# Kernel optimization log

Measured on AMD Instinct MI355X. Metric: run time of the kernel, lower is better.

The kernel has to match this reference:

```python
import jax, jax.numpy as jnp
import numpy as np
from jax import lax

B, H, W = 16, 256, 256
NUM_HIDDEN = 12
C = 3 + NUM_HIDDEN + 1  # 16 channels: rgb + hidden + alpha
HID = 64
ALPHA = 1.0
THR = 0.1

SOBEL_X = jnp.array([[-1.0, 0.0, 1.0], [-2.0, 0.0, 2.0], [-1.0, 0.0, 1.0]], jnp.float32) / 8.0
SOBEL_Y = jnp.array([[-1.0, -2.0, -1.0], [0.0, 0.0, 0.0], [1.0, 2.0, 1.0]], jnp.float32) / 8.0


def _sobel_conv(s, k):
    # s: [B,H,W] channel-summed state; k: [3,3]. SAME-padded 2D stencil.
    return lax.conv_general_dilated(
        s[..., None], k[:, :, None, None], window_strides=(1, 1), padding='SAME',
        dimension_numbers=('NHWC', 'HWIO', 'NHWC'))  # [B,H,W,1]


def _alive(x, thr):
    # 3x3 max-pool over alpha channel (index 3), SAME padding.
    a = x[..., 3:4]
    pooled = lax.reduce_window(a, -jnp.inf, lax.max, (1, 3, 3, 1), (1, 1, 1, 1), 'SAME')
    return pooled > thr  # [B,H,W,1] bool


def setup_inputs() -> dict:
    key = jax.random.key(0)
    ks = jax.random.split(key, 7)
    x = jax.random.uniform(ks[0], (B, H, W, C), dtype=jnp.float32)
    # UpdateNet params: 1x1 convs stored as dense matrices [in, out].
    w1 = jax.random.normal(ks[1], (3 * C, HID), dtype=jnp.float32) * (1.0 / np.sqrt(3 * C))
    b1 = jnp.zeros((HID,), jnp.float32)
    w2 = jax.random.normal(ks[2], (HID, HID), dtype=jnp.float32) * (1.0 / np.sqrt(HID))
    b2 = jnp.zeros((HID,), jnp.float32)
    # Original zero-inits w3; use small random values so outputs/grads are nontrivial.
    w3 = jax.random.normal(ks[3], (HID, C), dtype=jnp.float32) * 0.01
    return {'x': x, 'w1': w1, 'b1': b1, 'w2': w2, 'b2': b2, 'w3': w3}


def reference(x, w1, b1, w2, b2, w3):
    pre_life = _alive(x, THR)
    # Sobel perception: kernel[o,i] = sobel for all o,i  =>  each output channel
    # is the sobel filter applied to the channel-sum; broadcast across C channels.
    s = jnp.sum(x, axis=-1)                      # [B,H,W]
    sx = _sobel_conv(s, SOBEL_X)                 # [B,H,W,1]
    sy = _sobel_conv(s, SOBEL_Y)                 # [B,H,W,1]
    perc = jnp.concatenate(
        [x, jnp.broadcast_to(sx, x.shape), jnp.broadcast_to(sy, x.shape)], axis=-1)  # [B,H,W,3C]
    # UpdateNet: two biased 1x1 convs + ReLU, then unbiased 1x1 conv.
    h = jax.nn.relu(jnp.einsum('bhwi,io->bhwo', perc, w1) + b1)
    h = jax.nn.relu(jnp.einsum('bhwi,io->bhwo', h, w2) + b2)
    update = jnp.einsum('bhwi,io->bhwo', h, w3)  # [B,H,W,C]
    # cell_fire_rate == 1.0 -> stochastic update mask is all ones.
    x_new = x + ALPHA * update
    post_life = _alive(x_new, THR)
    life = (pre_life & post_life).astype(x_new.dtype)
    return x_new * life
```

## Files before the change

### kernel.cpp

```cpp
#include <hip/hip_runtime.h>
#include <hip/hip_bf16.h>
#include <cstdint>

#define NPIX (16 * 256 * 256)
#define THRV 0.1f

typedef __bf16 bf16x8 __attribute__((ext_vector_type(8)));
typedef float  f32x4  __attribute__((ext_vector_type(4)));

#define NSLOT 18

__global__ __launch_bounds__(256) void k_prep(const float* __restrict__ x,
                                              const float* __restrict__ w1,
                                              const float* __restrict__ b1,
                                              const float* __restrict__ w2,
                                              const float* __restrict__ b2,
                                              const float* __restrict__ w3,
                                              float2* __restrict__ hxs,
                                              unsigned char* __restrict__ rpre,
                                              float4* __restrict__ wpack) {
    __shared__ float sS[258];
    __shared__ float sA[258];
    const int tid = threadIdx.x;
    const int p = blockIdx.x * 256 + tid;

    const float4* xp = (const float4*)(x + (size_t)p * 16);
    float4 a = xp[0], b = xp[1], c = xp[2], d = xp[3];
    float sum = ((a.x + a.y) + (a.z + a.w)) + ((b.x + b.y) + (b.z + b.w)) +
                ((c.x + c.y) + (c.z + c.w)) + ((d.x + d.y) + (d.z + d.w));
    sS[tid + 1] = sum;
    sA[tid + 1] = a.w;
    if (tid == 0) { sS[0] = 0.f; sS[257] = 0.f; sA[0] = -1e30f; sA[257] = -1e30f; }
    __syncthreads();

    hxs[p] = make_float2(sS[tid + 2] - sS[tid],
                         sS[tid] + 2.f * sS[tid + 1] + sS[tid + 2]);
    float rm = fmaxf(sA[tid], fmaxf(sA[tid + 1], sA[tid + 2]));
    rpre[p] = (rm > THRV) ? 1 : 0;

    if (blockIdx.x == 0 && tid < 64) {
        const int lane = tid;
        const int r = lane & 15, g = lane >> 4;
#pragma unroll
        for (int n = 0; n < 4; ++n) {
            const int cc = n * 16 + r;
            bf16x8 f;
#pragma unroll
            for (int j = 0; j < 8; ++j) {
                float v = 0.f;
                if (j < 4) v = w1[(g * 4 + j) * 64 + cc];
                else if (g == 0 && j == 4) { for (int t = 0; t < 16; ++t) v += w1[(16 + t) * 64 + cc]; }
                else if (g == 0 && j == 5) { for (int t = 0; t < 16; ++t) v += w1[(32 + t) * 64 + cc]; }
                else if (g == 1 && j == 4) v = b1[cc];
                f[j] = (__bf16)v;
            }
            wpack[n * 64 + lane] = *(const float4*)&f;
        }
#pragma unroll
        for (int s = 0; s < 2; ++s)
#pragma unroll
            for (int n = 0; n < 4; ++n) {
                bf16x8 f;
#pragma unroll
                for (int j = 0; j < 8; ++j) {
                    const int psi = (2 * s + (j >> 2)) * 16 + g * 4 + (j & 3);
                    f[j] = (__bf16)w2[psi * 64 + n * 16 + r];
                }
                wpack[(4 + s * 4 + n) * 64 + lane] = *(const float4*)&f;
            }
#pragma unroll
        for (int s = 0; s < 2; ++s) {
            bf16x8 f;
#pragma unroll
            for (int j = 0; j < 8; ++j) {
                const int psi = (2 * s + (j >> 2)) * 16 + g * 4 + (j & 3);
                f[j] = (__bf16)w3[psi * 16 + r];
            }
            wpack[(12 + s) * 64 + lane] = *(const float4*)&f;
        }
#pragma unroll
        for (int n = 0; n < 4; ++n) {
            f32x4 v;
#pragma unroll
            for (int q = 0; q < 4; ++q) v[q] = b2[n * 16 + g * 4 + q];
            wpack[(14 + n) * 64 + lane] = *(const float4*)&v;
        }
    }
}

__global__ __launch_bounds__(256) void k_mfma(const float* __restrict__ x,
                                              const float2* __restrict__ hxs,
                                              const float4* __restrict__ wpack,
                                              float* __restrict__ out,
                                              unsigned char* __restrict__ anewf) {
    const int tid = threadIdx.x;
    const int wv = tid >> 6, lane = tid & 63;
    const int r = lane & 15, g = lane >> 4;

    bf16x8 w1f[4], w2f[2][4], w3f[2];
    f32x4 b2v[4];
#pragma unroll
    for (int n = 0; n < 4; ++n) { float4 t = wpack[n * 64 + lane]; w1f[n] = *(bf16x8*)&t; }
#pragma unroll
    for (int s2 = 0; s2 < 2; ++s2)
#pragma unroll
        for (int n = 0; n < 4; ++n) { float4 t = wpack[(4 + s2 * 4 + n) * 64 + lane]; w2f[s2][n] = *(bf16x8*)&t; }
#pragma unroll
    for (int s2 = 0; s2 < 2; ++s2) { float4 t = wpack[(12 + s2) * 64 + lane]; w3f[s2] = *(bf16x8*)&t; }
#pragma unroll
    for (int n = 0; n < 4; ++n) { float4 t = wpack[(14 + n) * 64 + lane]; b2v[n] = *(f32x4*)&t; }

    const int row = (blockIdx.x & 7) * 512 + (blockIdx.x >> 3);
    const int y = row & 255;
    const size_t rbase = (size_t)row * 256;
    const int wcol = wv * 64;

    const int y2 = y + g - 1;
    const bool gok = (g < 3) & ((unsigned)y2 < 256u);
    const size_t hbase = ((rbase >> 8) << 8) * 1 + ((size_t)(row >> 8) << 16);
    const float2* hrow = hxs + ((size_t)(row >> 8) << 16) + (size_t)(gok ? y2 : 0) * 256;

    float4 xf[4]; float2 hv[4];
#pragma unroll
    for (int t = 0; t < 4; ++t) {
        const int col = wcol + t * 16 + r;
        xf[t] = *(const float4*)(x + (rbase + col) * 16 + g * 4);
        hv[t] = gok ? hrow[col] : make_float2(0.f, 0.f);
    }

#pragma unroll
    for (int t = 0; t < 4; ++t) {
        const int col = wcol + t * 16 + r;
        const size_t pix = rbase + col;

        float ax = hv[t].x * ((g == 1) ? 2.f : 1.f);
        float ay = (g == 2) ? hv[t].y : ((g == 0) ? -hv[t].y : 0.f);
        ax += __shfl_xor(ax, 16); ax += __shfl_xor(ax, 32);
        ay += __shfl_xor(ay, 16); ay += __shfl_xor(ay, 32);
        const float gx = ax * 0.125f;
        const float gy = ay * 0.125f;

        bf16x8 a1;
        a1[0] = (__bf16)xf[t].x; a1[1] = (__bf16)xf[t].y;
        a1[2] = (__bf16)xf[t].z; a1[3] = (__bf16)xf[t].w;
        a1[4] = (__bf16)(g == 0 ? gx : (g == 1 ? 1.f : 0.f));
        a1[5] = (__bf16)(g == 0 ? gy : 0.f);
        a1[6] = (__bf16)0.f; a1[7] = (__bf16)0.f;

        f32x4 acc1[4];
#pragma unroll
        for (int n = 0; n < 4; ++n)
            acc1[n] = __builtin_amdgcn_mfma_f32_16x16x32_bf16(
                w1f[n], a1, (f32x4){0.f, 0.f, 0.f, 0.f}, 0, 0, 0);

        bf16x8 bf2[2];
#pragma unroll
        for (int s2 = 0; s2 < 2; ++s2)
#pragma unroll
            for (int j = 0; j < 4; ++j) {
                bf2[s2][j]     = (__bf16)fmaxf(acc1[2 * s2][j], 0.f);
                bf2[s2][4 + j] = (__bf16)fmaxf(acc1[2 * s2 + 1][j], 0.f);
            }

        f32x4 acc2[4];
#pragma unroll
        for (int n = 0; n < 4; ++n) {
            acc2[n] = b2v[n];
            acc2[n] = __builtin_amdgcn_mfma_f32_16x16x32_bf16(w2f[0][n], bf2[0], acc2[n], 0, 0, 0);
            acc2[n] = __builtin_amdgcn_mfma_f32_16x16x32_bf16(w2f[1][n], bf2[1], acc2[n], 0, 0, 0);
        }

        bf16x8 bf3[2];
#pragma unroll
        for (int s2 = 0; s2 < 2; ++s2)
#pragma unroll
            for (int j = 0; j < 4; ++j) {
                bf3[s2][j]     = (__bf16)fmaxf(acc2[2 * s2][j], 0.f);
                bf3[s2][4 + j] = (__bf16)fmaxf(acc2[2 * s2 + 1][j], 0.f);
            }

        f32x4 acc3 = __builtin_amdgcn_mfma_f32_16x16x32_bf16(
            w3f[0], bf3[0], (f32x4){0.f, 0.f, 0.f, 0.f}, 0, 0, 0);
        acc3 = __builtin_amdgcn_mfma_f32_16x16x32_bf16(w3f[1], bf3[1], acc3, 0, 0, 0);

        f32x4 xn;
        xn[0] = xf[t].x + acc3[0]; xn[1] = xf[t].y + acc3[1];
        xn[2] = xf[t].z + acc3[2]; xn[3] = xf[t].w + acc3[3];
        __builtin_nontemporal_store(xn, (f32x4*)(out + pix * 16 + g * 4));
        if (g == 0) anewf[pix] = (xn[3] > THRV) ? 1 : 0;
    }
}

__global__ __launch_bounds__(256) void k_post(const unsigned char* __restrict__ rpre,
                                              const unsigned char* __restrict__ anewf,
                                              float* __restrict__ out) {
    const int q = blockIdx.x * 256 + threadIdx.x;
    const int p0 = q * 4;
    const int bi = p0 >> 16;
    const int rem = p0 & 65535;
    const int y = rem >> 8;
    const int c0 = rem & 255;
    const unsigned char* pr = rpre + ((size_t)bi << 16);
    const unsigned char* an = anewf + ((size_t)bi << 16);

    unsigned pre = 0, M = 0, l = 0, rr = 0;
#pragma unroll
    for (int dy = -1; dy <= 1; ++dy) {
        const int y2 = y + dy;
        if ((unsigned)y2 >= 256u) continue;
        const int ro = y2 * 256;
        pre |= *(const unsigned*)(pr + ro + c0);
        M   |= *(const unsigned*)(an + ro + c0);
        l   |= (c0 > 0)   ? (unsigned)an[ro + c0 - 1] : 0u;
        rr  |= (c0 < 252) ? (unsigned)an[ro + c0 + 4] : 0u;
    }
    const unsigned post = M | (M << 8) | l | (M >> 8) | (rr << 24);
    const unsigned alive = pre & post;
    if (alive != 0x01010101u) {
        const f32x4 z = (f32x4){0.f, 0.f, 0.f, 0.f};
#pragma unroll
        for (int i = 0; i < 4; ++i)
            if (!((alive >> (8 * i)) & 1u)) {
                f32x4* op = (f32x4*)(out + (size_t)(p0 + i) * 16);
                op[0] = z; op[1] = z; op[2] = z; op[3] = z;
            }
    }
}

extern "C" void kernel_launch(void* const* d_in, const int* in_sizes, int n_in,
                              void* d_out, int out_size, void* d_ws, size_t ws_size,
                              hipStream_t stream) {
    const float* x  = (const float*)d_in[0];
    const float* w1 = (const float*)d_in[1];
    const float* b1 = (const float*)d_in[2];
    const float* w2 = (const float*)d_in[3];
    const float* b2 = (const float*)d_in[4];
    const float* w3 = (const float*)d_in[5];
    float* out = (float*)d_out;

    float2* hxs = (float2*)d_ws;
    unsigned char* rpre  = (unsigned char*)(hxs + NPIX);
    unsigned char* anewf = rpre + NPIX;
    float4* wpack = (float4*)(anewf + NPIX);

    hipLaunchKernelGGL(k_prep, dim3(NPIX / 256), dim3(256), 0, stream,
                       x, w1, b1, w2, b2, w3, hxs, rpre, wpack);
    hipLaunchKernelGGL(k_mfma, dim3(NPIX / 256), dim3(256), 0, stream,
                       x, hxs, wpack, out, anewf);
    hipLaunchKernelGGL(k_post, dim3(NPIX / 1024), dim3(256), 0, stream,
                       rpre, anewf, out);
}
```

Measured before the change: 49.04 us.

## Fuse channel-sum prep into MFMA kernel with per-row flag handoff between blocks

Replaces the separate prep kernel with a single fused kernel in which blocks first publish channel sums and pre-alpha bits for one row, then run the MLP for a row shifted by two, spin-waiting on per-row ready flags for the neighbouring rows. The Sobel horizontal pass moves into the consumer, and the pre-life horizontal max moves into k_post, so the intermediate is one float per pixel instead of two. A tiny pack kernel writes the weights and clears the flags. This removes a kernel boundary and some intermediate traffic, but it relies on blocks being scheduled roughly in order for forward progress, and it drops the earlier row-interleaved block order.

```diff
diff --git a/kernel.cpp b/kernel.cpp
--- a/kernel.cpp
+++ b/kernel.cpp
@@ -3,42 +3,23 @@
 #include <cstdint>
 
 #define NPIX (16 * 256 * 256)
+#define NROWS 4096
 #define THRV 0.1f
+#define NSLOT 18
 
 typedef __bf16 bf16x8 __attribute__((ext_vector_type(8)));
 typedef float  f32x4  __attribute__((ext_vector_type(4)));
 
-#define NSLOT 18
-
-__global__ __launch_bounds__(256) void k_prep(const float* __restrict__ x,
-                                              const float* __restrict__ w1,
+__global__ __launch_bounds__(256) void k_pack(const float* __restrict__ w1,
                                               const float* __restrict__ b1,
                                               const float* __restrict__ w2,
                                               const float* __restrict__ b2,
                                               const float* __restrict__ w3,
-                                              float2* __restrict__ hxs,
-                                              unsigned char* __restrict__ rpre,
-                                              float4* __restrict__ wpack) {
-    __shared__ float sS[258];
-    __shared__ float sA[258];
+                                              float4* __restrict__ wpack,
+                                              unsigned* __restrict__ flags) {
     const int tid = threadIdx.x;
-    const int p = blockIdx.x * 256 + tid;
-
-    const float4* xp = (const float4*)(x + (size_t)p * 16);
-    float4 a = xp[0], b = xp[1], c = xp[2], d = xp[3];
-    float sum = ((a.x + a.y) + (a.z + a.w)) + ((b.x + b.y) + (b.z + b.w)) +
-                ((c.x + c.y) + (c.z + c.w)) + ((d.x + d.y) + (d.z + d.w));
-    sS[tid + 1] = sum;
-    sA[tid + 1] = a.w;
-    if (tid == 0) { sS[0] = 0.f; sS[257] = 0.f; sA[0] = -1e30f; sA[257] = -1e30f; }
-    __syncthreads();
-
-    hxs[p] = make_float2(sS[tid + 2] - sS[tid],
-                         sS[tid] + 2.f * sS[tid + 1] + sS[tid + 2]);
-    float rm = fmaxf(sA[tid], fmaxf(sA[tid + 1], sA[tid + 2]));
-    rpre[p] = (rm > THRV) ? 1 : 0;
-
-    if (blockIdx.x == 0 && tid < 64) {
+    for (int i = tid; i < NROWS; i += 256) flags[i] = 0u;
+    if (tid < 64) {
         const int lane = tid;
         const int r = lane & 15, g = lane >> 4;
 #pragma unroll
@@ -88,12 +69,32 @@
     }
 }
 
-__global__ __launch_bounds__(256) void k_mfma(const float* __restrict__ x,
-                                              const float2* __restrict__ hxs,
-                                              const float4* __restrict__ wpack,
-                                              float* __restrict__ out,
-                                              unsigned char* __restrict__ anewf) {
+__global__ __launch_bounds__(256) void k_fused(const float* __restrict__ x,
+                                               const float4* __restrict__ wpack,
+                                               float* __restrict__ s,
+                                               unsigned char* __restrict__ apre,
+                                               unsigned* __restrict__ flags,
+                                               float* __restrict__ out,
+                                               unsigned char* __restrict__ anewf) {
     const int tid = threadIdx.x;
+    const int bid = blockIdx.x;
+
+    if (bid < NROWS) {
+        const int p = bid * 256 + tid;
+        const float4* xp = (const float4*)(x + (size_t)p * 16);
+        float4 a = xp[0], b = xp[1], c = xp[2], d = xp[3];
+        float sum = ((a.x + a.y) + (a.z + a.w)) + ((b.x + b.y) + (b.z + b.w)) +
+                    ((c.x + c.y) + (c.z + c.w)) + ((d.x + d.y) + (d.z + d.w));
+        __hip_atomic_store(&s[p], sum, __ATOMIC_RELAXED, __HIP_MEMORY_SCOPE_AGENT);
+        apre[p] = (a.w > THRV) ? 1 : 0;
+        __syncthreads();
+        if (tid == 0)
+            __hip_atomic_store(&flags[bid], 1u, __ATOMIC_RELEASE, __HIP_MEMORY_SCOPE_AGENT);
+    }
+    if (bid < 2) return;
+
+    const int rm = bid - 2;
+    const int y = rm & 255;
     const int wv = tid >> 6, lane = tid & 63;
     const int r = lane & 15, g = lane >> 4;
 
@@ -110,22 +111,36 @@
 #pragma unroll
     for (int n = 0; n < 4; ++n) { float4 t = wpack[(14 + n) * 64 + lane]; b2v[n] = *(f32x4*)&t; }
 
-    const int row = (blockIdx.x & 7) * 512 + (blockIdx.x >> 3);
-    const int y = row & 255;
-    const size_t rbase = (size_t)row * 256;
+    if (tid == 0) {
+        while (!__hip_atomic_load(&flags[rm], __ATOMIC_RELAXED, __HIP_MEMORY_SCOPE_AGENT))
+            __builtin_amdgcn_s_sleep(2);
+        if (y > 0)
+            while (!__hip_atomic_load(&flags[rm - 1], __ATOMIC_RELAXED, __HIP_MEMORY_SCOPE_AGENT))
+                __builtin_amdgcn_s_sleep(2);
+        if (y < 255)
+            while (!__hip_atomic_load(&flags[rm + 1], __ATOMIC_RELAXED, __HIP_MEMORY_SCOPE_AGENT))
+                __builtin_amdgcn_s_sleep(2);
+    }
+    __syncthreads();
+
+    const size_t rbase = (size_t)rm * 256;
     const int wcol = wv * 64;
-
-    const int y2 = y + g - 1;
-    const bool gok = (g < 3) & ((unsigned)y2 < 256u);
-    const size_t hbase = ((rbase >> 8) << 8) * 1 + ((size_t)(row >> 8) << 16);
-    const float2* hrow = hxs + ((size_t)(row >> 8) << 16) + (size_t)(gok ? y2 : 0) * 256;
-
-    float4 xf[4]; float2 hv[4];
+    const int grow = rm + g - 1;
+    const bool gok = (g < 3) & ((unsigned)(y + g - 1) < 256u);
+
+    float4 xf[4];
+    float c0[4], c1[4], c2[4];
 #pragma unroll
     for (int t = 0; t < 4; ++t) {
-        const int col = wcol + t * 16 + r;
-        xf[t] = *(const float4*)(x + (rbase + col) * 16 + g * 4);
-        hv[t] = gok ? hrow[col] : make_float2(0.f, 0.f);
+        const int xc = wcol + t * 16 + r;
+        xf[t] = *(const float4*)(x + (rbase + xc) * 16 + g * 4);
+        const size_t sb = (size_t)grow * 256;
+        c0[t] = (gok && xc > 0)
+                    ? __hip_atomic_load(&s[sb + xc - 1], __ATOMIC_RELAXED, __HIP_MEMORY_SCOPE_AGENT) : 0.f;
+        c1[t] = gok
+                    ? __hip_atomic_load(&s[sb + xc], __ATOMIC_RELAXED, __HIP_MEMORY_SCOPE_AGENT) : 0.f;
+        c2[t] = (gok && xc < 255)
+                    ? __hip_atomic_load(&s[sb + xc + 1], __ATOMIC_RELAXED, __HIP_MEMORY_SCOPE_AGENT) : 0.f;
     }
 
 #pragma unroll
@@ -133,12 +148,12 @@
         const int col = wcol + t * 16 + r;
         const size_t pix = rbase + col;
 
-        float ax = hv[t].x * ((g == 1) ? 2.f : 1.f);
-        float ay = (g == 2) ? hv[t].y : ((g == 0) ? -hv[t].y : 0.f);
-        ax += __shfl_xor(ax, 16); ax += __shfl_xor(ax, 32);
-        ay += __shfl_xor(ay, 16); ay += __shfl_xor(ay, 32);
-        const float gx = ax * 0.125f;
-        const float gy = ay * 0.125f;
+        float px = (c2[t] - c0[t]) * ((g == 1) ? 2.f : 1.f);
+        float py = (float)(g - 1) * (c0[t] + 2.f * c1[t] + c2[t]);
+        px += __shfl_xor(px, 16); px += __shfl_xor(px, 32);
+        py += __shfl_xor(py, 16); py += __shfl_xor(py, 32);
+        const float gx = px * 0.125f;
+        const float gy = py * 0.125f;
 
         bf16x8 a1;
         a1[0] = (__bf16)xf[t].x; a1[1] = (__bf16)xf[t].y;
@@ -191,7 +206,7 @@
     }
 }
 
-__global__ __launch_bounds__(256) void k_post(const unsigned char* __restrict__ rpre,
+__global__ __launch_bounds__(256) void k_post(const unsigned char* __restrict__ apre,
                                               const unsigned char* __restrict__ anewf,
                                               float* __restrict__ out) {
     const int q = blockIdx.x * 256 + threadIdx.x;
@@ -200,20 +215,23 @@
     const int rem = p0 & 65535;
     const int y = rem >> 8;
     const int c0 = rem & 255;
-    const unsigned char* pr = rpre + ((size_t)bi << 16);
+    const unsigned char* pr = apre + ((size_t)bi << 16);
     const unsigned char* an = anewf + ((size_t)bi << 16);
 
-    unsigned pre = 0, M = 0, l = 0, rr = 0;
+    unsigned pM = 0, pl = 0, prr = 0, M = 0, l = 0, rr = 0;
 #pragma unroll
     for (int dy = -1; dy <= 1; ++dy) {
         const int y2 = y + dy;
         if ((unsigned)y2 >= 256u) continue;
         const int ro = y2 * 256;
-        pre |= *(const unsigned*)(pr + ro + c0);
+        pM  |= *(const unsigned*)(pr + ro + c0);
+        pl  |= (c0 > 0)   ? (unsigned)pr[ro + c0 - 1] : 0u;
+        prr |= (c0 < 252) ? (unsigned)pr[ro + c0 + 4] : 0u;
         M   |= *(const unsigned*)(an + ro + c0);
         l   |= (c0 > 0)   ? (unsigned)an[ro + c0 - 1] : 0u;
         rr  |= (c0 < 252) ? (unsigned)an[ro + c0 + 4] : 0u;
     }
+    const unsigned pre  = pM | (pM << 8) | pl | (pM >> 8) | (prr << 24);
     const unsigned post = M | (M << 8) | l | (M >> 8) | (rr << 24);
     const unsigned alive = pre & post;
     if (alive != 0x01010101u) {
@@ -238,15 +256,16 @@
     const float* w3 = (const float*)d_in[5];
     float* out = (float*)d_out;
 
-    float2* hxs = (float2*)d_ws;
-    unsigned char* rpre  = (unsigned char*)(hxs + NPIX);
-    unsigned char* anewf = rpre + NPIX;
+    float* s = (float*)d_ws;
+    unsigned char* apre  = (unsigned char*)(s + NPIX);
+    unsigned char* anewf = apre + NPIX;
     float4* wpack = (float4*)(anewf + NPIX);
-
-    hipLaunchKernelGGL(k_prep, dim3(NPIX / 256), dim3(256), 0, stream,
-                       x, w1, b1, w2, b2, w3, hxs, rpre, wpack);
-    hipLaunchKernelGGL(k_mfma, dim3(NPIX / 256), dim3(256), 0, stream,
-                       x, hxs, wpack, out, anewf);
+    unsigned* flags = (unsigned*)(wpack + NSLOT * 64);
+
+    hipLaunchKernelGGL(k_pack, dim3(1), dim3(256), 0, stream,
+                       w1, b1, w2, b2, w3, wpack, flags);
+    hipLaunchKernelGGL(k_fused, dim3(NROWS + 2), dim3(256), 0, stream,
+                       x, wpack, s, apre, flags, out, anewf);
     hipLaunchKernelGGL(k_post, dim3(NPIX / 1024), dim3(256), 0, stream,
-                       rpre, anewf, out);
-}
+                       apre, anewf, out);
+}
```

Result: slower. 160.8 us (+227.9%).
